# Optimization experiments

Measured on AMD Instinct MI355X. Metric: run time of the kernel, lower is better.

The kernel has to match this reference:

```python
import jax, jax.numpy as jnp
import numpy as np

# bitsandbytes FP4 code table (magnitudes), signed -> 16 codes (two zeros, harmless)
_FP4_MAGS = np.array([0.0, 0.0052083333, 1.0/6.0, 0.25, 1.0/3.0, 0.5, 2.0/3.0, 1.0], dtype=np.float32)
_FP4_CODES = np.sort(np.concatenate([-_FP4_MAGS, _FP4_MAGS])).astype(np.float32)
_FP4_BOUNDS = ((_FP4_CODES[:-1] + _FP4_CODES[1:]) * 0.5).astype(np.float32)
_BLOCK = 64  # bnb default FP4 blocksize


def fp4_roundtrip(w):
    """Simulate bnb quantize_fp4 -> dequantize_fp4 (blockwise absmax + nearest FP4 code)."""
    shp = w.shape
    wf = w.reshape(-1, _BLOCK)                              # [n_blocks, 64]
    absmax = jnp.max(jnp.abs(wf), axis=1, keepdims=True)    # per-block scale
    n = wf / jnp.maximum(absmax, 1e-12)                     # normalized to [-1, 1]
    idx = jnp.searchsorted(jnp.asarray(_FP4_BOUNDS), n)     # nearest-code index
    deq = jnp.asarray(_FP4_CODES)[idx] * absmax             # dequantized values
    return deq.reshape(shp)


def setup_inputs() -> dict:
    key = jax.random.key(0)
    k1, k2 = jax.random.split(key)
    in_features, out_features, tokens = 4096, 11008, 8192
    x = jax.random.normal(k1, (tokens, in_features), dtype=jnp.float32)
    weight = jax.random.normal(k2, (out_features, in_features), dtype=jnp.float32) * 0.1
    bias = jnp.zeros((out_features,), dtype=jnp.float32)
    return {"x": x, "weight": weight, "bias": bias}


def reference(x, weight, bias):
    # forward path with quantized weights: dequantize FP4 then matmul + bias
    w = fp4_roundtrip(weight)                # [out, in]
    return jnp.matmul(x, w.T) + bias         # [tokens, out]
```

## Files before the change

kernel.cpp:

```cpp
#include <hip/hip_runtime.h>
#include <hip/hip_bf16.h>
#include <stdint.h>

#define M_DIM 8192
#define N_DIM 11008
#define K_DIM 4096

typedef __attribute__((ext_vector_type(8))) short bf16x8;
typedef __attribute__((ext_vector_type(4))) float f32x4;

__device__ const float kCodes[16] = {
    -1.0f, -(float)(2.0 / 3.0), -0.5f, -(float)(1.0 / 3.0), -0.25f,
    -(float)(1.0 / 6.0), -0.0052083333f, -0.0f,
    0.0f, 0.0052083333f, (float)(1.0 / 6.0), 0.25f,
    (float)(1.0 / 3.0), 0.5f, (float)(2.0 / 3.0), 1.0f};

__device__ __forceinline__ float fp4_bound(int i) {
  return (kCodes[i] + kCodes[i + 1]) * 0.5f;
}

__device__ __forceinline__ unsigned short f2bf(float f) {
  uint32_t u = __float_as_uint(f);
  u = (u + 0x7FFFu + ((u >> 16) & 1u)) >> 16;
  return (unsigned short)u;
}

__device__ __forceinline__ float fp4_rt(float w, float d, float am) {
  float n = w / d;
  int idx = 0;
#pragma unroll
  for (int i = 0; i < 15; ++i) idx += (n > fp4_bound(i)) ? 1 : 0;
  return kCodes[idx] * am;
}

__global__ void quant_fp4_kernel(const float* __restrict__ W,
                                 unsigned short* __restrict__ Wq) {
  int t = blockIdx.x * 256 + threadIdx.x;
  size_t base = (size_t)t * 4;
  float4 v = *reinterpret_cast<const float4*>(W + base);
  float am = fmaxf(fmaxf(fabsf(v.x), fabsf(v.y)), fmaxf(fabsf(v.z), fabsf(v.w)));
  am = fmaxf(am, __shfl_xor(am, 1));
  am = fmaxf(am, __shfl_xor(am, 2));
  am = fmaxf(am, __shfl_xor(am, 4));
  am = fmaxf(am, __shfl_xor(am, 8));
  float d = fmaxf(am, 1e-12f);
  ushort4 o;
  o.x = f2bf(fp4_rt(v.x, d, am));
  o.y = f2bf(fp4_rt(v.y, d, am));
  o.z = f2bf(fp4_rt(v.z, d, am));
  o.w = f2bf(fp4_rt(v.w, d, am));
  *reinterpret_cast<ushort4*>(Wq + base) = o;
}

__device__ __forceinline__ uint32_t pack2(float lo, float hi) {
  return (uint32_t)f2bf(lo) | ((uint32_t)f2bf(hi) << 16);
}

__global__ void cast_bf16_kernel(const float* __restrict__ X,
                                 uint32_t* __restrict__ Y) {
  int t = blockIdx.x * 256 + threadIdx.x;
  size_t base = (size_t)t * 8;
  float4 a = *reinterpret_cast<const float4*>(X + base);
  float4 b = *reinterpret_cast<const float4*>(X + base + 4);
  uint4 o;
  o.x = pack2(a.x, a.y);
  o.y = pack2(a.z, a.w);
  o.z = pack2(b.x, b.y);
  o.w = pack2(b.z, b.w);
  *reinterpret_cast<uint4*>(Y + (size_t)t * 4) = o;
}

#define GLOAD(src, dst)                                                        \
  __builtin_amdgcn_global_load_lds(                                           \
      (const __attribute__((address_space(1))) void*)(src),                   \
      (__attribute__((address_space(3))) void*)(dst), 16, 0, 0)

#define WAIT_LGKM4()                                                           \
  asm volatile("s_waitcnt lgkmcnt(4)" ::: "memory");                           \
  __builtin_amdgcn_sched_barrier(0);                                           \
  __builtin_amdgcn_s_setprio(1);

#define WAIT_LGKM8()                                                           \
  asm volatile("s_waitcnt lgkmcnt(8)" ::: "memory");                           \
  __builtin_amdgcn_sched_barrier(0);                                           \
  __builtin_amdgcn_s_setprio(1);

#define ENDBAR()                                                               \
  __builtin_amdgcn_s_setprio(0);                                               \
  __builtin_amdgcn_sched_barrier(0);                                           \
  __builtin_amdgcn_s_barrier();

#define ENDBAR_VM0()                                                           \
  __builtin_amdgcn_s_setprio(0);                                               \
  __builtin_amdgcn_sched_barrier(0);                                           \
  asm volatile("s_waitcnt vmcnt(0)" ::: "memory");                             \
  __builtin_amdgcn_s_barrier();

__global__ __launch_bounds__(512, 2) void gemm256_kernel(
    const short* __restrict__ A, const short* __restrict__ B,
    const float* __restrict__ bias, float* __restrict__ C) {
  __shared__ short lds[2][4][8192];

  const int tid = threadIdx.x;
  const int wave = tid >> 6;
  const int lane = tid & 63;
  const int l15 = lane & 15;
  const int q4 = lane >> 4;
  const int wm = wave >> 2;
  const int wn = wave & 3;

  const int bid = blockIdx.x;
  const int g = bid & 7;
  const int idx = bid >> 3;
  const int brow = (g * 4 + (idx & 3)) * 256;
  const int bcol = (idx >> 2) * 256;

  const int srow = tid >> 3;
  const int scol = ((tid & 7) ^ ((tid >> 3) & 7)) << 3;
  const short* Asrc = A + (size_t)(brow + srow) * K_DIM + scol;
  const short* Bsrc = B + (size_t)(bcol + srow) * K_DIM + scol;
  const int wu0 = wave * 512;
  const int wu1 = 4096 + wave * 512;

  auto stageA = [&](int buf, int half, int t) {
    const short* s = Asrc + (size_t)half * 128 * K_DIM + t * 64;
    GLOAD(s, &lds[buf][half][wu0]);
    GLOAD(s + (size_t)64 * K_DIM, &lds[buf][half][wu1]);
  };
  auto stageB = [&](int buf, int half, int t) {
    const short* s = Bsrc + (size_t)half * 128 * K_DIM + t * 64;
    GLOAD(s, &lds[buf][2 + half][wu0]);
    GLOAD(s + (size_t)64 * K_DIM, &lds[buf][2 + half][wu1]);
  };

  const int offk0 = ((q4 ^ (l15 & 7)) << 4);
  const int offk1 = offk0 ^ 64;
  const char* aP[2] = {(const char*)&lds[0][wm][0] + l15 * 128,
                       (const char*)&lds[1][wm][0] + l15 * 128};
  const char* bP[2] = {
      (const char*)&lds[0][2 + (wn >> 1)][0] + (wn & 1) * 8192 + l15 * 128,
      (const char*)&lds[1][2 + (wn >> 1)][0] + (wn & 1) * 8192 + l15 * 128};

  f32x4 acc[8][4] = {};
  bf16x8 afA[4], afB[4], bfA[4], bfB[4];

  stageB(0, 0, 0);
  stageB(0, 1, 0);
  stageA(0, 0, 0);
  stageA(0, 1, 0);
  stageB(1, 0, 1);
  asm volatile("s_waitcnt vmcnt(2)" ::: "memory");
  __builtin_amdgcn_s_barrier();
#pragma unroll
  for (int m = 0; m < 4; ++m) afA[m] = *(const bf16x8*)(aP[0] + m * 2048 + offk0);
#pragma unroll
  for (int n = 0; n < 4; ++n) bfA[n] = *(const bf16x8*)(bP[0] + n * 2048 + offk0);

  for (int i = 0; i < 32; ++i) {
    const int t1 = 2 * i + 1;
    const int t2 = (2 * i + 2 < 64) ? 2 * i + 2 : 63;
    const int t3 = (2 * i + 3 < 64) ? 2 * i + 3 : 63;

#pragma unroll
    for (int m = 0; m < 4; ++m)
      afB[m] = *(const bf16x8*)(aP[0] + (4 + m) * 2048 + offk0);
    stageB(1, 1, t1);
    WAIT_LGKM4();
#pragma unroll
    for (int m = 0; m < 4; ++m)
#pragma unroll
      for (int n = 0; n < 4; ++n)
        acc[m][n] = __builtin_amdgcn_mfma_f32_16x16x32_bf16(afA[m], bfA[n],
                                                            acc[m][n], 0, 0, 0);
    ENDBAR();

#pragma unroll
    for (int m = 0; m < 4; ++m)
      afA[m] = *(const bf16x8*)(aP[0] + m * 2048 + offk1);
#pragma unroll
    for (int n = 0; n < 4; ++n)
      bfB[n] = *(const bf16x8*)(bP[0] + n * 2048 + offk1);
    stageA(1, 0, t1);
    stageA(1, 1, t1);
    WAIT_LGKM8();
#pragma unroll
    for (int m = 0; m < 4; ++m)
#pragma unroll
      for (int n = 0; n < 4; ++n)
        acc[4 + m][n] = __builtin_amdgcn_mfma_f32_16x16x32_bf16(
            afB[m], bfA[n], acc[4 + m][n], 0, 0, 0);
    ENDBAR();

#pragma unroll
    for (int m = 0; m < 4; ++m)
      afB[m] = *(const bf16x8*)(aP[0] + (4 + m) * 2048 + offk1);
    WAIT_LGKM4();
#pragma unroll
    for (int m = 0; m < 4; ++m)
#pragma unroll
      for (int n = 0; n < 4; ++n)
        acc[m][n] = __builtin_amdgcn_mfma_f32_16x16x32_bf16(afA[m], bfB[n],
                                                            acc[m][n], 0, 0, 0);
    ENDBAR_VM0();

#pragma unroll
    for (int m = 0; m < 4; ++m)
      afA[m] = *(const bf16x8*)(aP[1] + m * 2048 + offk0);
#pragma unroll
    for (int n = 0; n < 4; ++n)
      bfA[n] = *(const bf16x8*)(bP[1] + n * 2048 + offk0);
    stageB(0, 0, t2);
    WAIT_LGKM8();
#pragma unroll
    for (int m = 0; m < 4; ++m)
#pragma unroll
      for (int n = 0; n < 4; ++n)
        acc[4 + m][n] = __builtin_amdgcn_mfma_f32_16x16x32_bf16(
            afB[m], bfB[n], acc[4 + m][n], 0, 0, 0);
    ENDBAR();

#pragma unroll
    for (int m = 0; m < 4; ++m)
      afB[m] = *(const bf16x8*)(aP[1] + (4 + m) * 2048 + offk0);
    stageB(0, 1, t2);
    WAIT_LGKM4();
#pragma unroll
    for (int m = 0; m < 4; ++m)
#pragma unroll
      for (int n = 0; n < 4; ++n)
        acc[m][n] = __builtin_amdgcn_mfma_f32_16x16x32_bf16(afA[m], bfA[n],
                                                            acc[m][n], 0, 0, 0);
    ENDBAR();

#pragma unroll
    for (int m = 0; m < 4; ++m)
      afA[m] = *(const bf16x8*)(aP[1] + m * 2048 + offk1);
#pragma unroll
    for (int n = 0; n < 4; ++n)
      bfB[n] = *(const bf16x8*)(bP[1] + n * 2048 + offk1);
    stageA(0, 0, t2);
    stageA(0, 1, t2);
    WAIT_LGKM8();
#pragma unroll
    for (int m = 0; m < 4; ++m)
#pragma unroll
      for (int n = 0; n < 4; ++n)
        acc[4 + m][n] = __builtin_amdgcn_mfma_f32_16x16x32_bf16(
            afB[m], bfA[n], acc[4 + m][n], 0, 0, 0);
    ENDBAR();

#pragma unroll
    for (int m = 0; m < 4; ++m)
      afB[m] = *(const bf16x8*)(aP[1] + (4 + m) * 2048 + offk1);
    WAIT_LGKM4();
#pragma unroll
    for (int m = 0; m < 4; ++m)
#pragma unroll
      for (int n = 0; n < 4; ++n)
        acc[m][n] = __builtin_amdgcn_mfma_f32_16x16x32_bf16(afA[m], bfB[n],
                                                            acc[m][n], 0, 0, 0);
    ENDBAR_VM0();

#pragma unroll
    for (int m = 0; m < 4; ++m)
      afA[m] = *(const bf16x8*)(aP[0] + m * 2048 + offk0);
#pragma unroll
    for (int n = 0; n < 4; ++n)
      bfA[n] = *(const bf16x8*)(bP[0] + n * 2048 + offk0);
    stageB(1, 0, t3);
    WAIT_LGKM8();
#pragma unroll
    for (int m = 0; m < 4; ++m)
#pragma unroll
      for (int n = 0; n < 4; ++n)
        acc[4 + m][n] = __builtin_amdgcn_mfma_f32_16x16x32_bf16(
            afB[m], bfB[n], acc[4 + m][n], 0, 0, 0);
    ENDBAR();
  }

  const int crow0 = brow + wm * 128 + q4 * 4;
  const int ccol0 = bcol + wn * 64 + l15;
#pragma unroll
  for (int n = 0; n < 4; ++n) {
    const float bv = bias[ccol0 + n * 16];
#pragma unroll
    for (int m = 0; m < 8; ++m) {
      const size_t rb = (size_t)(crow0 + m * 16) * N_DIM + (ccol0 + n * 16);
#pragma unroll
      for (int j = 0; j < 4; ++j) C[rb + (size_t)j * N_DIM] = acc[m][n][j] + bv;
    }
  }
}

extern "C" void kernel_launch(void* const* d_in, const int* in_sizes, int n_in,
                              void* d_out, int out_size, void* d_ws, size_t ws_size,
                              hipStream_t stream) {
  const float* x = (const float*)d_in[0];
  const float* w = (const float*)d_in[1];
  const float* bias = (const float*)d_in[2];
  float* out = (float*)d_out;

  unsigned short* wq = (unsigned short*)d_ws;
  unsigned short* xb = wq + (size_t)N_DIM * K_DIM;

  {
    int nt = N_DIM * K_DIM / 4;
    quant_fp4_kernel<<<nt / 256, 256, 0, stream>>>(w, wq);
  }
  {
    int nt = M_DIM * K_DIM / 8;
    cast_bf16_kernel<<<nt / 256, 256, 0, stream>>>(x, (uint32_t*)xb);
  }
  {
    gemm256_kernel<<<dim3(1376), 512, 0, stream>>>((const short*)xb,
                                                   (const short*)wq, bias, out);
  }
}
```

Before: 750.5 us.

## Merge prep kernels and split GEMM tail into a separate 128x128 kernel

Fuses the FP4 weight quantization and the activation bf16 cast into one launch that dispatches on block index. The main 256-tile GEMM now covers only the first 1280 tiles (N columns up to 10240). A new simple single-buffered 128x128 GEMM kernel handles the remaining 768 columns with 384 blocks, so the last partial wave of large tiles becomes a finer-grained tail. The tail kernel runs in sequence after the main one and is not pipelined, which risks leaving the GPU underfilled during it.

```diff
diff --git a/kernel.cpp b/kernel.cpp
--- a/kernel.cpp
+++ b/kernel.cpp
@@ -5,6 +5,8 @@
 #define M_DIM 8192
 #define N_DIM 11008
 #define K_DIM 4096
+#define NQB 44032
+#define NCB 16384
 
 typedef __attribute__((ext_vector_type(8))) short bf16x8;
 typedef __attribute__((ext_vector_type(4))) float f32x4;
@@ -33,41 +35,44 @@
   return kCodes[idx] * am;
 }
 
-__global__ void quant_fp4_kernel(const float* __restrict__ W,
-                                 unsigned short* __restrict__ Wq) {
-  int t = blockIdx.x * 256 + threadIdx.x;
-  size_t base = (size_t)t * 4;
-  float4 v = *reinterpret_cast<const float4*>(W + base);
-  float am = fmaxf(fmaxf(fabsf(v.x), fabsf(v.y)), fmaxf(fabsf(v.z), fabsf(v.w)));
-  am = fmaxf(am, __shfl_xor(am, 1));
-  am = fmaxf(am, __shfl_xor(am, 2));
-  am = fmaxf(am, __shfl_xor(am, 4));
-  am = fmaxf(am, __shfl_xor(am, 8));
-  float d = fmaxf(am, 1e-12f);
-  ushort4 o;
-  o.x = f2bf(fp4_rt(v.x, d, am));
-  o.y = f2bf(fp4_rt(v.y, d, am));
-  o.z = f2bf(fp4_rt(v.z, d, am));
-  o.w = f2bf(fp4_rt(v.w, d, am));
-  *reinterpret_cast<ushort4*>(Wq + base) = o;
-}
-
 __device__ __forceinline__ uint32_t pack2(float lo, float hi) {
   return (uint32_t)f2bf(lo) | ((uint32_t)f2bf(hi) << 16);
 }
 
-__global__ void cast_bf16_kernel(const float* __restrict__ X,
-                                 uint32_t* __restrict__ Y) {
-  int t = blockIdx.x * 256 + threadIdx.x;
-  size_t base = (size_t)t * 8;
-  float4 a = *reinterpret_cast<const float4*>(X + base);
-  float4 b = *reinterpret_cast<const float4*>(X + base + 4);
-  uint4 o;
-  o.x = pack2(a.x, a.y);
-  o.y = pack2(a.z, a.w);
-  o.z = pack2(b.x, b.y);
-  o.w = pack2(b.z, b.w);
-  *reinterpret_cast<uint4*>(Y + (size_t)t * 4) = o;
+__global__ void prep_kernel(const float* __restrict__ W,
+                            unsigned short* __restrict__ Wq,
+                            const float* __restrict__ X,
+                            uint32_t* __restrict__ Y) {
+  const int bid = blockIdx.x;
+  if (bid < NQB) {
+    int t = bid * 256 + threadIdx.x;
+    size_t base = (size_t)t * 4;
+    float4 v = *reinterpret_cast<const float4*>(W + base);
+    float am =
+        fmaxf(fmaxf(fabsf(v.x), fabsf(v.y)), fmaxf(fabsf(v.z), fabsf(v.w)));
+    am = fmaxf(am, __shfl_xor(am, 1));
+    am = fmaxf(am, __shfl_xor(am, 2));
+    am = fmaxf(am, __shfl_xor(am, 4));
+    am = fmaxf(am, __shfl_xor(am, 8));
+    float d = fmaxf(am, 1e-12f);
+    ushort4 o;
+    o.x = f2bf(fp4_rt(v.x, d, am));
+    o.y = f2bf(fp4_rt(v.y, d, am));
+    o.z = f2bf(fp4_rt(v.z, d, am));
+    o.w = f2bf(fp4_rt(v.w, d, am));
+    *reinterpret_cast<ushort4*>(Wq + base) = o;
+  } else {
+    int t = (bid - NQB) * 256 + threadIdx.x;
+    size_t base = (size_t)t * 8;
+    float4 a = *reinterpret_cast<const float4*>(X + base);
+    float4 b = *reinterpret_cast<const float4*>(X + base + 4);
+    uint4 o;
+    o.x = pack2(a.x, a.y);
+    o.y = pack2(a.z, a.w);
+    o.z = pack2(b.x, b.y);
+    o.w = pack2(b.z, b.w);
+    *reinterpret_cast<uint4*>(Y + (size_t)t * 4) = o;
+  }
 }
 
 #define GLOAD(src, dst)                                                        \
@@ -75,13 +80,8 @@
       (const __attribute__((address_space(1))) void*)(src),                   \
       (__attribute__((address_space(3))) void*)(dst), 16, 0, 0)
 
-#define WAIT_LGKM4()                                                           \
-  asm volatile("s_waitcnt lgkmcnt(4)" ::: "memory");                           \
-  __builtin_amdgcn_sched_barrier(0);                                           \
-  __builtin_amdgcn_s_setprio(1);
-
-#define WAIT_LGKM8()                                                           \
-  asm volatile("s_waitcnt lgkmcnt(8)" ::: "memory");                           \
+#define WAIT_LGKM(N)                                                           \
+  asm volatile("s_waitcnt lgkmcnt(" #N ")" ::: "memory");                      \
   __builtin_amdgcn_sched_barrier(0);                                           \
   __builtin_amdgcn_s_setprio(1);
 
@@ -165,7 +165,7 @@
     for (int m = 0; m < 4; ++m)
       afB[m] = *(const bf16x8*)(aP[0] + (4 + m) * 2048 + offk0);
     stageB(1, 1, t1);
-    WAIT_LGKM4();
+    WAIT_LGKM(4);
 #pragma unroll
     for (int m = 0; m < 4; ++m)
 #pragma unroll
@@ -182,7 +182,7 @@
       bfB[n] = *(const bf16x8*)(bP[0] + n * 2048 + offk1);
     stageA(1, 0, t1);
     stageA(1, 1, t1);
-    WAIT_LGKM8();
+    WAIT_LGKM(8);
 #pragma unroll
     for (int m = 0; m < 4; ++m)
 #pragma unroll
@@ -194,7 +194,7 @@
 #pragma unroll
     for (int m = 0; m < 4; ++m)
       afB[m] = *(const bf16x8*)(aP[0] + (4 + m) * 2048 + offk1);
-    WAIT_LGKM4();
+    WAIT_LGKM(4);
 #pragma unroll
     for (int m = 0; m < 4; ++m)
 #pragma unroll
@@ -210,7 +210,7 @@
     for (int n = 0; n < 4; ++n)
       bfA[n] = *(const bf16x8*)(bP[1] + n * 2048 + offk0);
     stageB(0, 0, t2);
-    WAIT_LGKM8();
+    WAIT_LGKM(8);
 #pragma unroll
     for (int m = 0; m < 4; ++m)
 #pragma unroll
@@ -223,7 +223,7 @@
     for (int m = 0; m < 4; ++m)
       afB[m] = *(const bf16x8*)(aP[1] + (4 + m) * 2048 + offk0);
     stageB(0, 1, t2);
-    WAIT_LGKM4();
+    WAIT_LGKM(4);
 #pragma unroll
     for (int m = 0; m < 4; ++m)
 #pragma unroll
@@ -240,7 +240,7 @@
       bfB[n] = *(const bf16x8*)(bP[1] + n * 2048 + offk1);
     stageA(0, 0, t2);
     stageA(0, 1, t2);
-    WAIT_LGKM8();
+    WAIT_LGKM(8);
 #pragma unroll
     for (int m = 0; m < 4; ++m)
 #pragma unroll
@@ -252,7 +252,7 @@
 #pragma unroll
     for (int m = 0; m < 4; ++m)
       afB[m] = *(const bf16x8*)(aP[1] + (4 + m) * 2048 + offk1);
-    WAIT_LGKM4();
+    WAIT_LGKM(4);
 #pragma unroll
     for (int m = 0; m < 4; ++m)
 #pragma unroll
@@ -268,7 +268,7 @@
     for (int n = 0; n < 4; ++n)
       bfA[n] = *(const bf16x8*)(bP[0] + n * 2048 + offk0);
     stageB(1, 0, t3);
-    WAIT_LGKM8();
+    WAIT_LGKM(8);
 #pragma unroll
     for (int m = 0; m < 4; ++m)
 #pragma unroll
@@ -288,6 +288,78 @@
       const size_t rb = (size_t)(crow0 + m * 16) * N_DIM + (ccol0 + n * 16);
 #pragma unroll
       for (int j = 0; j < 4; ++j) C[rb + (size_t)j * N_DIM] = acc[m][n][j] + bv;
+    }
+  }
+}
+
+__global__ __launch_bounds__(256, 2) void gemm_bt_kernel(
+    const short* __restrict__ A, const short* __restrict__ B,
+    const float* __restrict__ bias, float* __restrict__ C) {
+  __shared__ short Alds[128 * 32];
+  __shared__ short Blds[128 * 32];
+
+  const int tid = threadIdx.x;
+  const int wave = tid >> 6;
+  const int lane = tid & 63;
+  const int wr = wave >> 1;
+  const int wc = wave & 1;
+
+  const int bid = blockIdx.x;
+  const int brow = (bid & 63) * 128;
+  const int bcol = (80 + (bid >> 6)) * 128;
+
+  const int tr = tid >> 2;
+  const int tc = (tid & 3) * 8;
+  const short* Ag = A + (size_t)(brow + tr) * K_DIM + tc;
+  const short* Bg = B + (size_t)(bcol + tr) * K_DIM + tc;
+
+  short* AldsW = &Alds[wave * 512];
+  short* BldsW = &Blds[wave * 512];
+
+  f32x4 acc[4][4] = {};
+
+  const int la = (lane & 15) * 32 + (lane >> 4) * 8;
+  const short* Ar = &Alds[(wr * 64) * 32 + la];
+  const short* Br = &Blds[(wc * 64) * 32 + la];
+
+  for (int k0 = 0; k0 < K_DIM; k0 += 32) {
+    GLOAD(Ag, AldsW);
+    GLOAD(Ag + (size_t)64 * K_DIM, AldsW + 2048);
+    GLOAD(Bg, BldsW);
+    GLOAD(Bg + (size_t)64 * K_DIM, BldsW + 2048);
+    __syncthreads();
+
+    bf16x8 af[4], bfr[4];
+#pragma unroll
+    for (int m = 0; m < 4; ++m)
+      af[m] = *reinterpret_cast<const bf16x8*>(Ar + m * 16 * 32);
+#pragma unroll
+    for (int n = 0; n < 4; ++n)
+      bfr[n] = *reinterpret_cast<const bf16x8*>(Br + n * 16 * 32);
+
+#pragma unroll
+    for (int m = 0; m < 4; ++m)
+#pragma unroll
+      for (int n = 0; n < 4; ++n)
+        acc[m][n] = __builtin_amdgcn_mfma_f32_16x16x32_bf16(af[m], bfr[n],
+                                                            acc[m][n], 0, 0, 0);
+
+    __syncthreads();
+    Ag += 32;
+    Bg += 32;
+  }
+
+  const int crow0 = brow + wr * 64 + (lane >> 4) * 4;
+  const int ccol0 = bcol + wc * 64 + (lane & 15);
+#pragma unroll
+  for (int n = 0; n < 4; ++n) {
+    const int cc = ccol0 + n * 16;
+    const float bv = bias[cc];
+#pragma unroll
+    for (int m = 0; m < 4; ++m) {
+      const size_t rbase = (size_t)(crow0 + m * 16) * N_DIM + cc;
+#pragma unroll
+      for (int j = 0; j < 4; ++j) C[rbase + (size_t)j * N_DIM] = acc[m][n][j] + bv;
     }
   }
 }
@@ -303,16 +375,9 @@
   unsigned short* wq = (unsigned short*)d_ws;
   unsigned short* xb = wq + (size_t)N_DIM * K_DIM;
 
-  {
-    int nt = N_DIM * K_DIM / 4;
-    quant_fp4_kernel<<<nt / 256, 256, 0, stream>>>(w, wq);
-  }
-  {
-    int nt = M_DIM * K_DIM / 8;
-    cast_bf16_kernel<<<nt / 256, 256, 0, stream>>>(x, (uint32_t*)xb);
-  }
-  {
-    gemm256_kernel<<<dim3(1376), 512, 0, stream>>>((const short*)xb,
-                                                   (const short*)wq, bias, out);
-  }
-}
+  prep_kernel<<<NQB + NCB, 256, 0, stream>>>(w, wq, x, (uint32_t*)xb);
+  gemm256_kernel<<<dim3(1280), 512, 0, stream>>>((const short*)xb,
+                                                 (const short*)wq, bias, out);
+  gemm_bt_kernel<<<dim3(384), 256, 0, stream>>>((const short*)xb,
+                                                (const short*)wq, bias, out);
+}
```

Result: no change. 761.9 us (+1.5%).
